# Kernel tuning notes

Measured on AMD Instinct MI355X. Metric: run time of the kernel, lower is better.

The kernel has to match this reference:

```python
import jax, jax.numpy as jnp
import numpy as np

N, T, L = 4, 2048, 2048
DQIN, DFEAT, DQK, DV = 32, 34, 64, 64  # modality feat=34 -> V input = 34-2 = 32, K input = last col


def _sorted_timeline(k, shape):
    return jnp.sort(jax.random.uniform(k, shape, jnp.float32) * 100.0, axis=-1)


def setup_inputs() -> dict:
    key = jax.random.key(0)
    ks = jax.random.split(key, 32)
    inp = {}
    inp["ref_data"] = jax.random.normal(ks[0], (N, 1, T, DQIN), jnp.float32)
    inp["ref_t"] = _sorted_timeline(ks[1], (N, 1, T))
    inp["m1_data"] = jax.random.normal(ks[2], (N, 1, L, DFEAT), jnp.float32)
    inp["m1_t"] = _sorted_timeline(ks[3], (N, 1, L))
    inp["m2_data"] = jax.random.normal(ks[4], (N, 1, L, DFEAT), jnp.float32)
    inp["m2_t"] = _sorted_timeline(ks[5], (N, 1, L))
    inp["m3_data"] = jax.random.normal(ks[6], (N, 1, L, DFEAT), jnp.float32)
    inp["m3_t"] = _sorted_timeline(ks[7], (N, 1, L))
    # shared W_Q (bias=False): d_q_in -> d_qk
    inp["Wq"] = jax.random.normal(ks[8], (DQIN, DQK), jnp.float32) / np.sqrt(DQIN)
    # per-modality params: W_K: 1 -> d_qk (with bias), W_V: (DFEAT-2) -> d_v (with bias), log-temperature
    for i, m in enumerate(["1", "2", "3"]):
        b = 9 + 4 * i
        inp["Wk" + m] = jax.random.normal(ks[b], (1, DQK), jnp.float32)
        inp["bk" + m] = jax.random.normal(ks[b + 1], (DQK,), jnp.float32) * 0.02
        inp["Wv" + m] = jax.random.normal(ks[b + 2], (DFEAT - 2, DV), jnp.float32) / np.sqrt(DFEAT - 2)
        inp["bv" + m] = jax.random.normal(ks[b + 3], (DV,), jnp.float32) * 0.02
        inp["log_tau" + m] = jnp.zeros((), jnp.float32)  # log(init_tau=1)
    return inp


def _unimodal(Q, ref_t, data, t, Wk, bk, Wv, bv, log_tau):
    # K path: last feature column through linear, then feature_map_k = [1, -x]
    Kr = data[..., -1:] @ Wk + bk                                   # (N,1,L,DQK)
    K = jnp.concatenate([jnp.ones(Kr.shape[:-1] + (1,), Kr.dtype), -Kr], axis=-1)  # (N,1,L,DQK+1)
    V = data[..., :-2] @ Wv + bv                                    # (N,1,L,DV)
    tau = jnp.exp(log_tau)
    # gaussian weight: -(Q.K)^2 / tau
    S = -jnp.square(jnp.einsum('nhtc,nhlc->nhtl', Q, K)) / tau       # (N,1,T,L)
    mask = (ref_t[..., :, None] >= t[..., None, :]).astype(S.dtype)  # (N,1,T,L)
    A = jax.nn.softmax(S * mask, axis=-1) * mask
    return jnp.einsum('nhtl,nhlc->nhtc', A, V)                       # (N,1,T,DV)


def reference(ref_data, ref_t, m1_data, m1_t, m2_data, m2_t, m3_data, m3_t,
              Wq, Wk1, bk1, Wv1, bv1, log_tau1, Wk2, bk2, Wv2, bv2, log_tau2,
              Wk3, bk3, Wv3, bv3, log_tau3):
    # compute_Q (qk_type='time'): Q = add_one(W_Q(ref_data)) -> append ones column
    Qr = jnp.einsum('nhtd,dk->nhtk', ref_data, Wq)
    Q = jnp.concatenate([Qr, jnp.ones(Qr.shape[:-1] + (1,), Qr.dtype)], axis=-1)  # (N,1,T,DQK+1)
    y1 = _unimodal(Q, ref_t, m1_data, m1_t, Wk1, bk1, Wv1, bv1, log_tau1)
    y2 = _unimodal(Q, ref_t, m2_data, m2_t, Wk2, bk2, Wv2, bv2, log_tau2)
    y3 = _unimodal(Q, ref_t, m3_data, m3_t, Wk3, bk3, Wv3, bv3, log_tau3)
    # original returns dict {m1: y1, m2: y2, m3: y3}; stacked here (3,N,1,T,DV)
    return jnp.stack([y1, y2, y3], axis=0)
```

## Files before the change

### kernel.cpp

```cpp
#include <hip/hip_runtime.h>

namespace {

typedef unsigned int uint;
typedef unsigned short ushort_t;
typedef __attribute__((ext_vector_type(8))) short bf16x8;
typedef __attribute__((ext_vector_type(4))) float f32x4;

constexpr int N = 4, T = 2048, L = 2048;
constexpr int DQIN = 32, DQK = 64;

constexpr int VI_SZ = 3 * N * 64 * L;
constexpr int X_SZ = 3 * N * L;
constexpr int A_SZ = 3 * N * T;

union PK8 { int i[4]; bf16x8 s; };

__global__ __launch_bounds__(256) void mm_prep(
    const float* __restrict__ ref_data, const float* __restrict__ ref_t,
    const float* __restrict__ d1, const float* __restrict__ t1,
    const float* __restrict__ d2, const float* __restrict__ t2,
    const float* __restrict__ d3, const float* __restrict__ t3,
    const float* __restrict__ Wq,
    const float* __restrict__ Wk1, const float* __restrict__ bk1,
    const float* __restrict__ Wv1, const float* __restrict__ bv1, const float* __restrict__ lt1,
    const float* __restrict__ Wk2, const float* __restrict__ bk2,
    const float* __restrict__ Wv2, const float* __restrict__ bv2, const float* __restrict__ lt2,
    const float* __restrict__ Wk3, const float* __restrict__ bk3,
    const float* __restrict__ Wv3, const float* __restrict__ bv3, const float* __restrict__ lt3,
    float* __restrict__ Aq, float* __restrict__ Gq, int* __restrict__ Cq,
    ushort_t* __restrict__ VI, float* __restrict__ X) {
  const int b = blockIdx.x;
  const int tid = threadIdx.x;

  if (b < 32) {
    const int idx = b * 256 + tid;
    __shared__ float sWq[DQIN * DQK];
    __shared__ float sWk[3][DQK];
    __shared__ float sbk[3][DQK];
    for (int i = tid; i < DQIN * DQK; i += 256) sWq[i] = Wq[i];
    if (tid < DQK) {
      sWk[0][tid] = Wk1[tid]; sbk[0][tid] = bk1[tid];
      sWk[1][tid] = Wk2[tid]; sbk[1][tid] = bk2[tid];
      sWk[2][tid] = Wk3[tid]; sbk[2][tid] = bk3[tid];
    }
    __syncthreads();
    float x[DQIN];
    const float* rp = ref_data + idx * DQIN;
#pragma unroll
    for (int i = 0; i < DQIN; i++) x[i] = rp[i];
    float qr[DQK];
#pragma unroll
    for (int j = 0; j < DQK; j += 4) {
      float4 acc4 = make_float4(0.f, 0.f, 0.f, 0.f);
#pragma unroll
      for (int i = 0; i < DQIN; i++) {
        const float4 w = *(const float4*)&sWq[i * DQK + j];
        acc4.x = fmaf(x[i], w.x, acc4.x);
        acc4.y = fmaf(x[i], w.y, acc4.y);
        acc4.z = fmaf(x[i], w.z, acc4.z);
        acc4.w = fmaf(x[i], w.w, acc4.w);
      }
      qr[j] = acc4.x; qr[j + 1] = acc4.y; qr[j + 2] = acc4.z; qr[j + 3] = acc4.w;
    }
    const float* lts[3] = {lt1, lt2, lt3};
#pragma unroll
    for (int m = 0; m < 3; m++) {
      const float rs = __expf(-0.5f * lts[m][0]);
      float g = 0.f, h = 0.f;
#pragma unroll
      for (int j = 1; j < DQK; j++) {
        g = fmaf(qr[j], sWk[m][j - 1], g);
        h = fmaf(qr[j], sbk[m][j - 1], h);
      }
      g += sWk[m][DQK - 1];
      h += sbk[m][DQK - 1];
      Aq[m * (N * T) + idx] = (qr[0] - h) * rs;
      Gq[m * (N * T) + idx] = g * rs;
    }
  } else if (b < 128) {
    const int sidx = (b - 32) * 256 + tid;
    const int m = sidx >> 13;
    const int nt = sidx & 8191;
    const int n = nt >> 11;
    const float rt = ref_t[nt];
    const float* tml = ((m == 0) ? t1 : (m == 1 ? t2 : t3)) + n * L;
    int lo = 0, hi = L;
    while (lo < hi) {
      const int mid = (lo + hi) >> 1;
      if (tml[mid] <= rt) lo = mid + 1; else hi = mid;
    }
    Cq[m * 8192 + nt] = lo;
  } else {
    const int vb = b - 128;
    const int mn = vb >> 7;
    const int m = mn >> 2, n = mn & 3;
    const int lseg = (vb & 127) * 16;
    const float* dm = (m == 0) ? d1 : (m == 1 ? d2 : d3);
    const float* Wv = (m == 0) ? Wv1 : (m == 1 ? Wv2 : Wv3);
    const float* bv = (m == 0) ? bv1 : (m == 1 ? bv2 : bv3);
    const int cdim = tid & 63;
    const int qq = tid >> 6;
    const int l0 = lseg + qq * 4;

    float Wc[32];
#pragma unroll
    for (int i = 0; i < 32; i++) Wc[i] = Wv[i * 64 + cdim];
    const float bvc = bv[cdim];

    uint hi16[4], lo16[4];
#pragma unroll
    for (int k = 0; k < 4; k++) {
      const float* dp = dm + (size_t)(n * L + l0 + k) * 34;
      float acc = bvc;
#pragma unroll
      for (int i = 0; i < 32; i += 2) {
        const float2 dd = *(const float2*)&dp[i];
        acc = fmaf(dd.x, Wc[i], acc);
        acc = fmaf(dd.y, Wc[i + 1], acc);
      }
      uint u = __float_as_uint(acc);
      uint h = (u + 0x7fffu + ((u >> 16) & 1u)) & 0xffff0000u;
      float res = acc - __uint_as_float(h);
      uint ul = __float_as_uint(res);
      uint hl = (ul + 0x7fffu + ((ul >> 16) & 1u)) >> 16;
      hi16[k] = h >> 16;
      lo16[k] = hl;
    }
    const int pkh0 = (int)(hi16[0] | (hi16[1] << 16));
    const int pkh1 = (int)(hi16[2] | (hi16[3] << 16));
    const int pkl0 = (int)(lo16[0] | (lo16[1] << 16));
    const int pkl1 = (int)(lo16[2] | (lo16[3] << 16));

    const int hh = cdim >> 5, ct = (cdim >> 4) & 1, m16f = cdim & 15;
    const int ch = l0 >> 6, wf = (l0 >> 5) & 1, qf = (l0 >> 3) & 3, half = (l0 >> 2) & 1;
    const int lanef = qf * 16 + m16f;
    ushort_t* dst = VI + (size_t)mn * 262144 + (size_t)ch * 8192 + wf * 4096 +
                    (hh * 2 + ct) * 1024 + lanef * 8 + half * 4;
    *(int2*)dst = make_int2(pkh0, pkh1);
    *(int2*)(dst + 512) = make_int2(pkl0, pkl1);

    if (tid < 16) {
      const int l = lseg + tid;
      X[mn * L + l] = dm[(size_t)(n * L + l) * 34 + 33];
    }
  }
}

__global__ __launch_bounds__(128, 4) void mm_attn_main(
    const ushort_t* __restrict__ VI, const float* __restrict__ X,
    const float* __restrict__ Aq, const float* __restrict__ Gq, const int* __restrict__ Cq,
    float* __restrict__ out) {
  __shared__ float sc[1152];

  const int b = blockIdx.x;
  const int mn = b % 12;
  const int rg = 127 - (b / 12);

  const int tid = threadIdx.x;
  const int lane = tid & 63;
  const int w = tid >> 6;
  const int q = lane >> 4;
  const int m16 = lane & 15;

  const int tbase = mn * T + rg * 16;

  const int c = Cq[tbase + m16];
  const int cmax = __shfl(c, 15, 64);
  const int cmin = __shfl(c, 0, 64);

  const float a = Aq[tbase + m16];
  const float g = Gq[tbase + m16];

  f32x4 acc[4];
#pragma unroll
  for (int i = 0; i < 4; i++) acc[i] = (f32x4){0.f, 0.f, 0.f, 0.f};
  float z = 0.f;

  const float* xg = X + mn * L;

  const ushort_t* pb[4];
#pragma unroll
  for (int hh = 0; hh < 2; hh++)
#pragma unroll
    for (int ct = 0; ct < 2; ct++)
      pb[hh * 2 + ct] = VI + (size_t)mn * 262144 + w * 4096 +
                        (hh * 2 + ct) * 1024 + lane * 8;

  const int nchw = (cmax > w * 32) ? ((cmax - w * 32 + 63) >> 6) : 0;

  float4 xa, xb;
  if (nchw > 0) {
    const int k0 = w * 32 + q * 8;
    xa = *(const float4*)&xg[k0];
    xb = *(const float4*)&xg[k0 + 4];
  }

  for (int ch = 0; ch < nchw; ch++) {
    const int kbase = (ch << 6) + w * 32;
    const int k0 = kbase + q * 8;
    const float4 cxa = xa, cxb = xb;
    if (ch + 1 < nchw) {
      xa = *(const float4*)&xg[k0 + 64];
      xb = *(const float4*)&xg[k0 + 68];
    }
    const float xs[8] = {cxa.x, cxa.y, cxa.z, cxa.w, cxb.x, cxb.y, cxb.z, cxb.w};
    float wv[8];
    if (kbase + 32 <= cmin) {
#pragma unroll
      for (int jj = 0; jj < 8; jj++) {
        const float d = fmaf(-g, xs[jj], a);
        wv[jj] = __expf(-d * d);
        z += wv[jj];
      }
    } else {
#pragma unroll
      for (int jj = 0; jj < 8; jj++) {
        const float d = fmaf(-g, xs[jj], a);
        const float e = __expf(-d * d);
        wv[jj] = (k0 + jj < c) ? e : 0.f;
        z += wv[jj];
      }
    }
    PK8 ph, pl;
#pragma unroll
    for (int p2 = 0; p2 < 4; p2++) {
      const uint u0 = __float_as_uint(wv[2 * p2]);
      const uint u1 = __float_as_uint(wv[2 * p2 + 1]);
      const uint h0 = u0 & 0xffff0000u, h1 = u1 & 0xffff0000u;
      const float l0f = wv[2 * p2] - __uint_as_float(h0);
      const float l1f = wv[2 * p2 + 1] - __uint_as_float(h1);
      ph.i[p2] = (int)((h0 >> 16) | h1);
      pl.i[p2] = (int)((__float_as_uint(l0f) >> 16) | (__float_as_uint(l1f) & 0xffff0000u));
    }
    const bf16x8 ahi = ph.s, alo = pl.s;
    const size_t choff = (size_t)ch * 8192;
#pragma unroll
    for (int hh = 0; hh < 2; hh++) {
#pragma unroll
      for (int ct = 0; ct < 2; ct++) {
        const ushort_t* p = pb[hh * 2 + ct] + choff;
        const bf16x8 bh = *(const bf16x8*)p;
        const bf16x8 bl = *(const bf16x8*)(p + 512);
        acc[hh * 2 + ct] =
            __builtin_amdgcn_mfma_f32_16x16x32_bf16(ahi, bh, acc[hh * 2 + ct], 0, 0, 0);
        acc[hh * 2 + ct] =
            __builtin_amdgcn_mfma_f32_16x16x32_bf16(ahi, bl, acc[hh * 2 + ct], 0, 0, 0);
        acc[hh * 2 + ct] =
            __builtin_amdgcn_mfma_f32_16x16x32_bf16(alo, bh, acc[hh * 2 + ct], 0, 0, 0);
      }
    }
  }

  z += __shfl_xor(z, 16, 64);
  z += __shfl_xor(z, 32, 64);

  const int ow = w ^ 1;
#pragma unroll
  for (int p = 0; p < 2; p++)
    *(f32x4*)&sc[((w * 2 + p) * 64 + lane) * 4] = acc[ow * 2 + p];
  sc[1024 + w * 64 + lane] = z;
  __syncthreads();
  const float zt = z + sc[1024 + ow * 64 + lane];
  f32x4 r[2];
#pragma unroll
  for (int p = 0; p < 2; p++)
    r[p] = acc[w * 2 + p] + *(const f32x4*)&sc[((ow * 2 + p) * 64 + lane) * 4];

#pragma unroll
  for (int rr = 0; rr < 4; rr++) {
    const int row = q * 4 + rr;
    const float zr = __shfl(zt, row, 64);
    const int cr = __shfl(c, row, 64);
    const float inv = 1.0f / (zr + (float)(L - cr));
#pragma unroll
    for (int p = 0; p < 2; p++) {
      out[(size_t)(tbase + row) * 64 + w * 32 + p * 16 + m16] = r[p][rr] * inv;
    }
  }
}

}

extern "C" void kernel_launch(void* const* d_in, const int* in_sizes, int n_in,
                              void* d_out, int out_size, void* d_ws, size_t ws_size,
                              hipStream_t stream) {
  const float* ref_data = (const float*)d_in[0];
  const float* ref_t = (const float*)d_in[1];
  const float* m1_data = (const float*)d_in[2];
  const float* m1_t = (const float*)d_in[3];
  const float* m2_data = (const float*)d_in[4];
  const float* m2_t = (const float*)d_in[5];
  const float* m3_data = (const float*)d_in[6];
  const float* m3_t = (const float*)d_in[7];
  const float* Wq = (const float*)d_in[8];
  const float* Wk1 = (const float*)d_in[9];
  const float* bk1 = (const float*)d_in[10];
  const float* Wv1 = (const float*)d_in[11];
  const float* bv1 = (const float*)d_in[12];
  const float* lt1 = (const float*)d_in[13];
  const float* Wk2 = (const float*)d_in[14];
  const float* bk2 = (const float*)d_in[15];
  const float* Wv2 = (const float*)d_in[16];
  const float* bv2 = (const float*)d_in[17];
  const float* lt2 = (const float*)d_in[18];
  const float* Wk3 = (const float*)d_in[19];
  const float* bk3 = (const float*)d_in[20];
  const float* Wv3 = (const float*)d_in[21];
  const float* bv3 = (const float*)d_in[22];
  const float* lt3 = (const float*)d_in[23];

  float* ws = (float*)d_ws;
  ushort_t* VI = (ushort_t*)ws;
  float* Xw = ws + VI_SZ;
  float* Aq = Xw + X_SZ;
  float* Gq = Aq + A_SZ;
  int* Cq = (int*)(Gq + A_SZ);

  mm_prep<<<dim3(1664), dim3(256), 0, stream>>>(
      ref_data, ref_t, m1_data, m1_t, m2_data, m2_t, m3_data, m3_t, Wq,
      Wk1, bk1, Wv1, bv1, lt1, Wk2, bk2, Wv2, bv2, lt2, Wk3, bk3, Wv3, bv3, lt3,
      Aq, Gq, Cq, VI, Xw);
  mm_attn_main<<<dim3(12 * 128), dim3(128), 0, stream>>>(
      VI, Xw, Aq, Gq, Cq, (float*)d_out);
}
```

Before: 146.0 us.

## Process two query row-groups per block with four waves sharing V tiles

Each block now handles 32 query rows (two 16-row groups) with four waves splitting the key dimension, so each loaded V fragment feeds MFMAs for both row groups. The block-to-work mapping is reshuffled so consecutive blocks spread across modality/batch slices, and partial accumulators from all four waves are reduced through shared memory. The intent is to halve V traffic per output row and improve load balance for the causal mask. The cost is more registers and shared memory per block, plus a larger cross-wave reduction.

```diff
diff --git a/kernel.cpp b/kernel.cpp
--- a/kernel.cpp
+++ b/kernel.cpp
@@ -147,82 +147,84 @@
   }
 }
 
-__global__ __launch_bounds__(128, 4) void mm_attn_main(
+__global__ __launch_bounds__(256, 3) void mm_attn_main(
     const ushort_t* __restrict__ VI, const float* __restrict__ X,
     const float* __restrict__ Aq, const float* __restrict__ Gq, const int* __restrict__ Cq,
     float* __restrict__ out) {
-  __shared__ float sc[1152];
+  __shared__ float sacc[4][8][64][4];
+  __shared__ float sz[4][2][64];
 
   const int b = blockIdx.x;
-  const int mn = b % 12;
-  const int rg = 127 - (b / 12);
+  const int x = b & 7;
+  const int s = b >> 3;
+  const int wid = x * 96 + s;
+  const int mn = wid >> 6;
+  const int pj = 63 - (wid & 63);
 
   const int tid = threadIdx.x;
+  const int ww = tid >> 6;
   const int lane = tid & 63;
-  const int w = tid >> 6;
   const int q = lane >> 4;
   const int m16 = lane & 15;
 
-  const int tbase = mn * T + rg * 16;
-
-  const int c = Cq[tbase + m16];
-  const int cmax = __shfl(c, 15, 64);
-  const int cmin = __shfl(c, 0, 64);
-
-  const float a = Aq[tbase + m16];
-  const float g = Gq[tbase + m16];
-
-  f32x4 acc[4];
-#pragma unroll
-  for (int i = 0; i < 4; i++) acc[i] = (f32x4){0.f, 0.f, 0.f, 0.f};
-  float z = 0.f;
+  const int tbase0 = mn * T + (pj * 2) * 16;
+  const int tbase1 = tbase0 + 16;
+
+  const int c0 = Cq[tbase0 + m16];
+  const int c1 = Cq[tbase1 + m16];
+  const int cmin0 = __shfl(c0, 0, 64);
+  const int cmin1 = __shfl(c1, 0, 64);
+  const int cmax0 = __shfl(c0, 15, 64);
+  const int cmaxP = __shfl(c1, 15, 64);
+
+  const float a0 = Aq[tbase0 + m16], g0 = Gq[tbase0 + m16];
+  const float a1 = Aq[tbase1 + m16], g1 = Gq[tbase1 + m16];
+
+  f32x4 acc[8];
+#pragma unroll
+  for (int i = 0; i < 8; i++) acc[i] = (f32x4){0.f, 0.f, 0.f, 0.f};
+  float z0 = 0.f, z1 = 0.f;
 
   const float* xg = X + mn * L;
-
-  const ushort_t* pb[4];
-#pragma unroll
-  for (int hh = 0; hh < 2; hh++)
-#pragma unroll
-    for (int ct = 0; ct < 2; ct++)
-      pb[hh * 2 + ct] = VI + (size_t)mn * 262144 + w * 4096 +
-                        (hh * 2 + ct) * 1024 + lane * 8;
-
-  const int nchw = (cmax > w * 32) ? ((cmax - w * 32 + 63) >> 6) : 0;
+  const ushort_t* pbB = VI + (size_t)mn * 262144 + lane * 8;
+
+  const int nchw = (cmaxP > ww * 32) ? ((cmaxP - ww * 32 + 127) >> 7) : 0;
 
   float4 xa, xb;
   if (nchw > 0) {
-    const int k0 = w * 32 + q * 8;
+    const int k0 = ww * 32 + q * 8;
     xa = *(const float4*)&xg[k0];
     xb = *(const float4*)&xg[k0 + 4];
   }
 
   for (int ch = 0; ch < nchw; ch++) {
-    const int kbase = (ch << 6) + w * 32;
+    const int kbase = (ch << 7) + ww * 32;
     const int k0 = kbase + q * 8;
     const float4 cxa = xa, cxb = xb;
     if (ch + 1 < nchw) {
-      xa = *(const float4*)&xg[k0 + 64];
-      xb = *(const float4*)&xg[k0 + 68];
+      xa = *(const float4*)&xg[k0 + 128];
+      xb = *(const float4*)&xg[k0 + 132];
     }
     const float xs[8] = {cxa.x, cxa.y, cxa.z, cxa.w, cxb.x, cxb.y, cxb.z, cxb.w};
+
     float wv[8];
-    if (kbase + 32 <= cmin) {
+    if (kbase + 32 <= cmin1) {
 #pragma unroll
       for (int jj = 0; jj < 8; jj++) {
-        const float d = fmaf(-g, xs[jj], a);
+        const float d = fmaf(-g1, xs[jj], a1);
         wv[jj] = __expf(-d * d);
-        z += wv[jj];
+        z1 += wv[jj];
       }
     } else {
 #pragma unroll
       for (int jj = 0; jj < 8; jj++) {
-        const float d = fmaf(-g, xs[jj], a);
+        const float d = fmaf(-g1, xs[jj], a1);
         const float e = __expf(-d * d);
-        wv[jj] = (k0 + jj < c) ? e : 0.f;
-        z += wv[jj];
-      }
-    }
-    PK8 ph, pl;
+        wv[jj] = (k0 + jj < c1) ? e : 0.f;
+        z1 += wv[jj];
+      }
+    }
+    PK8 ph1, pl1;
 #pragma unroll
     for (int p2 = 0; p2 < 4; p2++) {
       const uint u0 = __float_as_uint(wv[2 * p2]);
@@ -230,52 +232,94 @@
       const uint h0 = u0 & 0xffff0000u, h1 = u1 & 0xffff0000u;
       const float l0f = wv[2 * p2] - __uint_as_float(h0);
       const float l1f = wv[2 * p2 + 1] - __uint_as_float(h1);
-      ph.i[p2] = (int)((h0 >> 16) | h1);
-      pl.i[p2] = (int)((__float_as_uint(l0f) >> 16) | (__float_as_uint(l1f) & 0xffff0000u));
-    }
-    const bf16x8 ahi = ph.s, alo = pl.s;
-    const size_t choff = (size_t)ch * 8192;
-#pragma unroll
-    for (int hh = 0; hh < 2; hh++) {
-#pragma unroll
-      for (int ct = 0; ct < 2; ct++) {
-        const ushort_t* p = pb[hh * 2 + ct] + choff;
-        const bf16x8 bh = *(const bf16x8*)p;
-        const bf16x8 bl = *(const bf16x8*)(p + 512);
-        acc[hh * 2 + ct] =
-            __builtin_amdgcn_mfma_f32_16x16x32_bf16(ahi, bh, acc[hh * 2 + ct], 0, 0, 0);
-        acc[hh * 2 + ct] =
-            __builtin_amdgcn_mfma_f32_16x16x32_bf16(ahi, bl, acc[hh * 2 + ct], 0, 0, 0);
-        acc[hh * 2 + ct] =
-            __builtin_amdgcn_mfma_f32_16x16x32_bf16(alo, bh, acc[hh * 2 + ct], 0, 0, 0);
+      ph1.i[p2] = (int)((h0 >> 16) | h1);
+      pl1.i[p2] = (int)((__float_as_uint(l0f) >> 16) | (__float_as_uint(l1f) & 0xffff0000u));
+    }
+    const bf16x8 ahi1 = ph1.s, alo1 = pl1.s;
+
+    const bool act0 = (kbase < cmax0);
+    bf16x8 ahi0 = ahi1, alo0 = alo1;
+    if (act0) {
+      if (kbase + 32 <= cmin0) {
+#pragma unroll
+        for (int jj = 0; jj < 8; jj++) {
+          const float d = fmaf(-g0, xs[jj], a0);
+          wv[jj] = __expf(-d * d);
+          z0 += wv[jj];
+        }
+      } else {
+#pragma unroll
+        for (int jj = 0; jj < 8; jj++) {
+          const float d = fmaf(-g0, xs[jj], a0);
+          const float e = __expf(-d * d);
+          wv[jj] = (k0 + jj < c0) ? e : 0.f;
+          z0 += wv[jj];
+        }
+      }
+      PK8 ph0, pl0;
+#pragma unroll
+      for (int p2 = 0; p2 < 4; p2++) {
+        const uint u0 = __float_as_uint(wv[2 * p2]);
+        const uint u1 = __float_as_uint(wv[2 * p2 + 1]);
+        const uint h0 = u0 & 0xffff0000u, h1 = u1 & 0xffff0000u;
+        const float l0f = wv[2 * p2] - __uint_as_float(h0);
+        const float l1f = wv[2 * p2 + 1] - __uint_as_float(h1);
+        ph0.i[p2] = (int)((h0 >> 16) | h1);
+        pl0.i[p2] = (int)((__float_as_uint(l0f) >> 16) | (__float_as_uint(l1f) & 0xffff0000u));
+      }
+      ahi0 = ph0.s; alo0 = pl0.s;
+    }
+
+    const size_t choff = (size_t)((ch << 1) + (ww >> 1)) * 8192 + (ww & 1) * 4096;
+#pragma unroll
+    for (int uq = 0; uq < 4; uq++) {
+      const ushort_t* p = pbB + uq * 1024 + choff;
+      const bf16x8 bh = *(const bf16x8*)p;
+      const bf16x8 bl = *(const bf16x8*)(p + 512);
+      acc[4 + uq] = __builtin_amdgcn_mfma_f32_16x16x32_bf16(ahi1, bh, acc[4 + uq], 0, 0, 0);
+      acc[4 + uq] = __builtin_amdgcn_mfma_f32_16x16x32_bf16(ahi1, bl, acc[4 + uq], 0, 0, 0);
+      acc[4 + uq] = __builtin_amdgcn_mfma_f32_16x16x32_bf16(alo1, bh, acc[4 + uq], 0, 0, 0);
+      if (act0) {
+        acc[uq] = __builtin_amdgcn_mfma_f32_16x16x32_bf16(ahi0, bh, acc[uq], 0, 0, 0);
+        acc[uq] = __builtin_amdgcn_mfma_f32_16x16x32_bf16(ahi0, bl, acc[uq], 0, 0, 0);
+        acc[uq] = __builtin_amdgcn_mfma_f32_16x16x32_bf16(alo0, bh, acc[uq], 0, 0, 0);
       }
     }
   }
 
-  z += __shfl_xor(z, 16, 64);
-  z += __shfl_xor(z, 32, 64);
-
-  const int ow = w ^ 1;
-#pragma unroll
-  for (int p = 0; p < 2; p++)
-    *(f32x4*)&sc[((w * 2 + p) * 64 + lane) * 4] = acc[ow * 2 + p];
-  sc[1024 + w * 64 + lane] = z;
+  z0 += __shfl_xor(z0, 16, 64);
+  z0 += __shfl_xor(z0, 32, 64);
+  z1 += __shfl_xor(z1, 16, 64);
+  z1 += __shfl_xor(z1, 32, 64);
+
+#pragma unroll
+  for (int u = 0; u < 8; u++)
+    *(f32x4*)&sacc[ww][u][lane][0] = acc[u];
+  sz[ww][0][lane] = z0;
+  sz[ww][1][lane] = z1;
   __syncthreads();
-  const float zt = z + sc[1024 + ow * 64 + lane];
-  f32x4 r[2];
-#pragma unroll
-  for (int p = 0; p < 2; p++)
-    r[p] = acc[w * 2 + p] + *(const f32x4*)&sc[((ow * 2 + p) * 64 + lane) * 4];
-
-#pragma unroll
-  for (int rr = 0; rr < 4; rr++) {
-    const int row = q * 4 + rr;
-    const float zr = __shfl(zt, row, 64);
-    const int cr = __shfl(c, row, 64);
-    const float inv = 1.0f / (zr + (float)(L - cr));
-#pragma unroll
-    for (int p = 0; p < 2; p++) {
-      out[(size_t)(tbase + row) * 64 + w * 32 + p * 16 + m16] = r[p][rr] * inv;
+
+#pragma unroll
+  for (int e = 0; e < 2; e++) {
+    const int u = ww * 2 + e;
+    const int rgl = u >> 2, quad = u & 3;
+    f32x4 r = (f32x4){0.f, 0.f, 0.f, 0.f};
+    float zt = 0.f;
+#pragma unroll
+    for (int v = 0; v < 4; v++) {
+      r += *(const f32x4*)&sacc[v][u][lane][0];
+      zt += sz[v][rgl][lane];
+    }
+    const int cc = rgl ? c1 : c0;
+    const int tb = rgl ? tbase1 : tbase0;
+    const int col = (quad >> 1) * 32 + (quad & 1) * 16 + m16;
+#pragma unroll
+    for (int rr = 0; rr < 4; rr++) {
+      const int row = q * 4 + rr;
+      const float zr = __shfl(zt, row, 64);
+      const int cr = __shfl(cc, row, 64);
+      const float inv = 1.0f / (zr + (float)(L - cr));
+      out[(size_t)(tb + row) * 64 + col] = r[rr] * inv;
     }
   }
 }
@@ -321,6 +365,6 @@
       ref_data, ref_t, m1_data, m1_t, m2_data, m2_t, m3_data, m3_t, Wq,
       Wk1, bk1, Wv1, bv1, lt1, Wk2, bk2, Wv2, bv2, lt2, Wk3, bk3, Wv3, bv3, lt3,
       Aq, Gq, Cq, VI, Xw);
-  mm_attn_main<<<dim3(12 * 128), dim3(128), 0, stream>>>(
+  mm_attn_main<<<dim3(12 * 64), dim3(256), 0, stream>>>(
       VI, Xw, Aq, Gq, Cq, (float*)d_out);
 }
```

Result: no change. 147.2 us (+0.8%).
